# Kernel optimization log

Hardware: AMD Instinct MI355X
Metric: run time of the kernel (lower is better)

## Reference

```python
import jax, jax.numpy as jnp
import numpy as np
import math

GROUPS = 32
EPS = 1e-5
NUM_HEADS = 8


def group_norm(x, gamma, beta):
    # x: [B, C, H, W]; normalize within each of GROUPS channel groups over (C/G, H, W)
    B, C, H, W = x.shape
    xg = x.reshape(B, GROUPS, C // GROUPS, H, W)
    mean = jnp.mean(xg, axis=(2, 3, 4), keepdims=True)
    var = jnp.var(xg, axis=(2, 3, 4), keepdims=True)
    xn = ((xg - mean) * jax.lax.rsqrt(var + EPS)).reshape(B, C, H, W)
    return xn * gamma[None, :, None, None] + beta[None, :, None, None]


def setup_inputs() -> dict:
    key = jax.random.key(0)
    ks = jax.random.split(key, 10)
    C = 512
    B, H, W = 2, 64, 64
    s = 1.0 / math.sqrt(C)
    return {
        "x": jax.random.normal(ks[0], (B, C, H, W), jnp.float32),
        "gamma": jnp.ones((C,), jnp.float32),
        "beta": jnp.zeros((C,), jnp.float32),
        "Wq": jax.random.normal(ks[1], (C, C), jnp.float32) * s,
        "bq": jax.random.normal(ks[2], (C,), jnp.float32) * 0.01,
        "Wk": jax.random.normal(ks[3], (C, C), jnp.float32) * s,
        "bk": jax.random.normal(ks[4], (C,), jnp.float32) * 0.01,
        "Wv": jax.random.normal(ks[5], (C, C), jnp.float32) * s,
        "bv": jax.random.normal(ks[6], (C,), jnp.float32) * 0.01,
        "Wo": jax.random.normal(ks[7], (C, C), jnp.float32) * s,
        "bo": jax.random.normal(ks[8], (C,), jnp.float32) * 0.01,
    }


def reference(x, gamma, beta, Wq, bq, Wk, bk, Wv, bv, Wo, bo):
    B, C, H, W = x.shape
    N = H * W
    hd = C // NUM_HEADS
    h = group_norm(x, gamma, beta)
    h = h.reshape(B, C, N).transpose(0, 2, 1)  # [B, N, C]
    # torch nn.Linear: y = x @ W.T + b
    q = (h @ Wq.T + bq).reshape(B, N, NUM_HEADS, hd)
    k = (h @ Wk.T + bk).reshape(B, N, NUM_HEADS, hd)
    v = (h @ Wv.T + bv).reshape(B, N, NUM_HEADS, hd)
    scale = 1.0 / math.sqrt(hd)
    attn = jnp.einsum('bihd,bjhd->bijh', q, k) * scale  # [B, N, N, heads]
    attn = jax.nn.softmax(attn, axis=2)
    o = jnp.einsum('bijh,bjhd->bihd', attn, v).reshape(B, N, C)
    o = o @ Wo.T + bo
    o = o.transpose(0, 2, 1).reshape(B, C, H, W)
    return x + o
```

## Files before the change

### kernel.cpp

```cpp
#include <hip/hip_runtime.h>
#include <cstdint>
#include <cstddef>

typedef __bf16 bf16x8 __attribute__((ext_vector_type(8)));
typedef float f32x4 __attribute__((ext_vector_type(4)));
typedef float f32x2 __attribute__((ext_vector_type(2)));
typedef float f32x16 __attribute__((ext_vector_type(16)));
typedef unsigned short ushort8 __attribute__((ext_vector_type(8)));
typedef unsigned u32x2 __attribute__((ext_vector_type(2)));
typedef float f4 __attribute__((ext_vector_type(4)));

__device__ __forceinline__ unsigned short f2bf(float f) {
    __bf16 b = (__bf16)f;
    return *(unsigned short*)&b;
}
__device__ __forceinline__ unsigned pk2bf(float a, float b) {
#if __has_builtin(__builtin_amdgcn_cvt_pk_bf16_f32)
    typedef __bf16 bf16x2v __attribute__((ext_vector_type(2)));
    bf16x2v r = __builtin_amdgcn_cvt_pk_bf16_f32(a, b);
    return *(unsigned*)&r;
#else
    __bf16 x = (__bf16)a, y = (__bf16)b;
    unsigned short ux = *(unsigned short*)&x, uy = *(unsigned short*)&y;
    return (unsigned)ux | ((unsigned)uy << 16);
#endif
}
__device__ __forceinline__ float bf2f(unsigned short u) {
    union { unsigned u; float f; } v; v.u = ((unsigned)u) << 16; return v.f;
}

#if __has_builtin(__builtin_amdgcn_exp2f)
#define EXP2(x) __builtin_amdgcn_exp2f(x)
#else
#define EXP2(x) exp2f(x)
#endif

#define GLL(g, l) __builtin_amdgcn_global_load_lds( \
    (__attribute__((address_space(1))) void*)(g), \
    (__attribute__((address_space(3))) void*)(l), 16, 0, 0)

#define CS 0.18033688011112042f

__global__ __launch_bounds__(256) void prep(
    const float* __restrict__ wq, const float* __restrict__ wk,
    const float* __restrict__ wv, const float* __restrict__ wo,
    unsigned short* __restrict__ wb,
    const float* __restrict__ x, float* __restrict__ part)
{
    const int bid = blockIdx.x;
    if (bid < 4096) {
        int i = bid * 256 + threadIdx.x;
        const float* src = (i < 262144) ? wq : (i < 524288) ? wk : (i < 786432) ? wv : wo;
        wb[i] = f2bf(src[i & 262143]);
        return;
    }
    const int idx = bid - 4096;
    const int q = idx & 3, bg = idx >> 2;
    const f4* xv = (const f4*)(x + (size_t)bg * 65536 + q * 16384);
    float s = 0.f, sq = 0.f;
    for (int i = threadIdx.x; i < 4096; i += 256) {
        f4 v = xv[i];
        s  += v.x + v.y + v.z + v.w;
        sq += v.x * v.x + v.y * v.y + v.z * v.z + v.w * v.w;
    }
    #pragma unroll
    for (int off = 32; off > 0; off >>= 1) {
        s  += __shfl_xor(s, off, 64);
        sq += __shfl_xor(sq, off, 64);
    }
    __shared__ float red[8];
    const int w = threadIdx.x >> 6, lane = threadIdx.x & 63;
    if (lane == 0) { red[w] = s; red[4 + w] = sq; }
    __syncthreads();
    if (threadIdx.x == 0) {
        part[(bg * 4 + q) * 2]     = red[0] + red[1] + red[2] + red[3];
        part[(bg * 4 + q) * 2 + 1] = red[4] + red[5] + red[6] + red[7];
    }
}

__global__ __launch_bounds__(256) void gn_apply(
    const float* __restrict__ x, const float* __restrict__ gamma,
    const float* __restrict__ beta, const float* __restrict__ part,
    unsigned short* __restrict__ h)
{
    const int q = blockIdx.x, bg = blockIdx.y;
    const int b = bg >> 5, g = bg & 31;
    float s = 0.f, sq = 0.f;
    #pragma unroll
    for (int j = 0; j < 4; ++j) {
        s  += part[(bg * 4 + j) * 2];
        sq += part[(bg * 4 + j) * 2 + 1];
    }
    const float mean = s * (1.f / 65536.f);
    const float rstd = rsqrtf(sq * (1.f / 65536.f) - mean * mean + 1e-5f);

    float gm[16], bt[16];
    #pragma unroll
    for (int c = 0; c < 16; ++c) {
        gm[c] = gamma[g * 16 + c] * rstd;
        bt[c] = beta[g * 16 + c];
    }
    const float* xg = x + (size_t)bg * 65536;
    const int n0 = q * 1024 + threadIdx.x * 4;
    float val[16][4];
    #pragma unroll
    for (int c = 0; c < 16; ++c) {
        f4 v = *(const f4*)&xg[(size_t)c * 4096 + n0];
        val[c][0] = (v.x - mean) * gm[c] + bt[c];
        val[c][1] = (v.y - mean) * gm[c] + bt[c];
        val[c][2] = (v.z - mean) * gm[c] + bt[c];
        val[c][3] = (v.w - mean) * gm[c] + bt[c];
    }
    #pragma unroll
    for (int nn = 0; nn < 4; ++nn) {
        ushort8 v0, v1;
        #pragma unroll
        for (int c = 0; c < 8; ++c)  v0[c]     = f2bf(val[c][nn]);
        #pragma unroll
        for (int c = 8; c < 16; ++c) v1[c - 8] = f2bf(val[c][nn]);
        unsigned short* dst = h + ((size_t)(b * 4096 + n0 + nn)) * 512 + g * 16;
        *(ushort8*)dst = v0;
        *(ushort8*)(dst + 8) = v1;
    }
}

template <int MODE, int BM>
__global__ __launch_bounds__(256, 2) void gemm_bt(
    const unsigned short* __restrict__ A,
    const unsigned short* __restrict__ Bt,
    const float* __restrict__ bias0,
    const float* __restrict__ bias1,
    const float* __restrict__ bias2,
    const float* __restrict__ resid,
    void* __restrict__ outp,
    unsigned short* __restrict__ kout,
    unsigned short* __restrict__ vtout,
    int M, int N, int K)
{
    constexpr int MT = BM / 32;
    __shared__ __attribute__((aligned(16))) unsigned short As[BM * 32];
    __shared__ __attribute__((aligned(16))) unsigned short Bs[128 * 32];
    const int t = threadIdx.x;
    const int w = t >> 6, lane = t & 63;
    const int l15 = lane & 15, l4 = lane >> 4;
    const int bm = blockIdx.y, bn = blockIdx.x;
    const int wm = (w >> 1) * (BM / 2), wn = (w & 1) * 64;

    f32x4 acc[MT][4] = {};

    const int srow = t >> 2;
    const int sc8  = (t & 3) * 8;

    const unsigned short* gA0 = A  + (size_t)(bm * BM + srow) * K + sc8;
    const unsigned short* gB0 = Bt + (size_t)(bn * 128 + srow) * K + sc8;
    const unsigned short* gB1 = gB0 + (size_t)64 * K;
    unsigned short* lA0 = &As[w * 512];
    unsigned short* lB0 = &Bs[w * 512];
    unsigned short* lB1 = &Bs[2048 + w * 512];

    for (int k0 = 0; k0 < K; k0 += 32) {
        __syncthreads();
        GLL(gA0 + k0, lA0);
        if (BM == 128) GLL(gA0 + (size_t)64 * K + k0, &As[2048 + w * 512]);
        GLL(gB0 + k0, lB0);
        GLL(gB1 + k0, lB1);
        __syncthreads();

        bf16x8 af[MT], bfr[4];
        #pragma unroll
        for (int mt = 0; mt < MT; ++mt)
            af[mt] = *(const bf16x8*)&As[(wm + mt * 16 + l15) * 32 + l4 * 8];
        #pragma unroll
        for (int nt = 0; nt < 4; ++nt)
            bfr[nt] = *(const bf16x8*)&Bs[(wn + nt * 16 + l15) * 32 + l4 * 8];
        #pragma unroll
        for (int mt = 0; mt < MT; ++mt)
            #pragma unroll
            for (int nt = 0; nt < 4; ++nt)
                acc[mt][nt] = __builtin_amdgcn_mfma_f32_16x16x32_bf16(
                    af[mt], bfr[nt], acc[mt][nt], 0, 0, 0);
    }

    if (MODE == 0) {
        unsigned short* qout = (unsigned short*)outp;
        #pragma unroll
        for (int nt = 0; nt < 4; ++nt) {
            int col = bn * 128 + wn + nt * 16 + l15;
            const float* bp = (col < 512) ? bias0 : (col < 1024) ? bias1 : bias2;
            float bv = bp[col & 511];
            if (col < 1024) {
                unsigned short* dst = (col < 512) ? qout : kout;
                int cc = col & 511;
                float sc = (col < 512) ? CS : 1.0f;
                #pragma unroll
                for (int mt = 0; mt < MT; ++mt)
                    #pragma unroll
                    for (int r = 0; r < 4; ++r) {
                        int row = bm * BM + wm + mt * 16 + l4 * 4 + r;
                        dst[(size_t)row * 512 + cc] = f2bf((acc[mt][nt][r] + bv) * sc);
                    }
            } else {
                int hd = col - 1024;
                #pragma unroll
                for (int mt = 0; mt < MT; ++mt) {
                    int m = bm * BM + wm + mt * 16 + l4 * 4;
                    int bb = m >> 12, n = m & 4095;
                    unsigned u0 = pk2bf(acc[mt][nt][0] + bv, acc[mt][nt][1] + bv);
                    unsigned u1 = pk2bf(acc[mt][nt][2] + bv, acc[mt][nt][3] + bv);
                    unsigned short* dst = vtout +
                        ((size_t)(bb * 8 + (hd >> 6)) * 64 + (hd & 63)) * 4096 + n;
                    *(u32x2*)dst = (u32x2){u0, u1};
                }
            }
        }
    } else {
        float* outF = (float*)outp;
        #pragma unroll
        for (int mt = 0; mt < MT; ++mt)
            #pragma unroll
            for (int nt = 0; nt < 4; ++nt)
                #pragma unroll
                for (int r = 0; r < 4; ++r) {
                    int c = bm * BM + wm + mt * 16 + l4 * 4 + r;
                    int m = bn * 128 + wn + nt * 16 + l15;
                    int b = m >> 12, n = m & 4095;
                    size_t idx = ((size_t)(b * 512 + c)) * 4096 + n;
                    outF[idx] = acc[mt][nt][r] + bias0[c] + resid[idx];
                }
    }
}

__global__ __launch_bounds__(256, 2) void attn_kernel(
    const unsigned short* __restrict__ qb, const unsigned short* __restrict__ kb,
    const unsigned short* __restrict__ vt,
    unsigned short* __restrict__ opart, float* __restrict__ lbuf)
{
    __shared__ __attribute__((aligned(16))) unsigned short Ks[64][72];
    __shared__ __attribute__((aligned(16))) unsigned short Vts[64][72];

    const int bh = blockIdx.y, b = bh >> 3, h = bh & 7;
    const int qbase = blockIdx.x * 256;
    const int s = blockIdx.z, ks0 = s * 2048;
    const int t = threadIdx.x, w = t >> 6, lane = t & 63;
    const int l31 = lane & 31, h5 = lane >> 5;

    const unsigned short* Qg = qb + ((size_t)(b * 4096 + qbase + w * 64)) * 512 + h * 64;
    const unsigned short* Kg = kb + ((size_t)(b * 4096 + ks0)) * 512 + h * 64;
    const unsigned short* Vg = vt + ((size_t)bh) * 64 * 4096 + ks0;

    bf16x8 qf[2][4];
    #pragma unroll
    for (int qt = 0; qt < 2; ++qt)
        #pragma unroll
        for (int kc = 0; kc < 4; ++kc)
            qf[qt][kc] = *(const bf16x8*)(Qg + (size_t)(qt * 32 + l31) * 512 + kc * 16 + h5 * 8);

    f32x16 Oacc[2][2] = {};
    float li[2] = {0.f, 0.f};

    const int sr = t >> 2, sc = (t & 3) * 16;
    const int grp = (sr >> 2) & 3;
    const int srcrow = (grp == 1) ? sr + 4 : (grp == 2) ? sr - 4 : sr;
    const unsigned short* gK = Kg + (size_t)srcrow * 512 + sc;
    const unsigned short* gV = Vg + (size_t)sr * 4096 + sc;
    unsigned short* lK = &Ks[sr][sc];
    unsigned short* lV = &Vts[sr][sc];

    ushort8 kr[2], vr[2];
    kr[0] = *(const ushort8*)(gK);
    kr[1] = *(const ushort8*)(gK + 8);
    vr[0] = *(const ushort8*)(gV);
    vr[1] = *(const ushort8*)(gV + 8);

    for (int kt = 0; kt < 32; ++kt) {
        __syncthreads();
        *(ushort8*)(lK)     = kr[0];
        *(ushort8*)(lK + 8) = kr[1];
        *(ushort8*)(lV)     = vr[0];
        *(ushort8*)(lV + 8) = vr[1];
        __syncthreads();
        if (kt < 31) {
            const unsigned short* nk = gK + (size_t)(kt + 1) * 64 * 512;
            const unsigned short* nv = gV + (kt + 1) * 64;
            kr[0] = *(const ushort8*)(nk);
            kr[1] = *(const ushort8*)(nk + 8);
            vr[0] = *(const ushort8*)(nv);
            vr[1] = *(const ushort8*)(nv + 8);
        }

        f32x16 St[2][2] = {};
        #pragma unroll
        for (int ct = 0; ct < 2; ++ct)
            #pragma unroll
            for (int kc = 0; kc < 4; ++kc) {
                bf16x8 kf = *(const bf16x8*)&Ks[ct * 32 + l31][kc * 16 + h5 * 8];
                St[0][ct] = __builtin_amdgcn_mfma_f32_32x32x16_bf16(kf, qf[0][kc], St[0][ct], 0, 0, 0);
                St[1][ct] = __builtin_amdgcn_mfma_f32_32x32x16_bf16(kf, qf[1][kc], St[1][ct], 0, 0, 0);
            }

        union PU { unsigned u[4]; bf16x8 v; };
        PU pf[2][4];
        #pragma unroll
        for (int qt = 0; qt < 2; ++qt) {
            f32x2 a2 = {0.f, 0.f};
            #pragma unroll
            for (int ct = 0; ct < 2; ++ct) {
                #pragma unroll
                for (int r = 0; r < 16; ++r)
                    St[qt][ct][r] = EXP2(St[qt][ct][r]);
                #pragma unroll
                for (int r = 0; r < 8; ++r) {
                    f32x2 p = {St[qt][ct][2 * r], St[qt][ct][2 * r + 1]};
                    a2 += p;
                }
                #pragma unroll
                for (int kkl = 0; kkl < 2; ++kkl)
                    #pragma unroll
                    for (int i = 0; i < 4; ++i)
                        pf[qt][ct * 2 + kkl].u[i] =
                            pk2bf(St[qt][ct][kkl * 8 + 2 * i], St[qt][ct][kkl * 8 + 2 * i + 1]);
            }
            li[qt] += a2[0] + a2[1];
        }

        #pragma unroll
        for (int kkl = 0; kkl < 4; ++kkl)
            #pragma unroll
            for (int dt = 0; dt < 2; ++dt) {
                bf16x8 vf = *(const bf16x8*)&Vts[dt * 32 + l31][kkl * 16 + h5 * 8];
                Oacc[dt][0] = __builtin_amdgcn_mfma_f32_32x32x16_bf16(vf, pf[0][kkl].v, Oacc[dt][0], 0, 0, 0);
                Oacc[dt][1] = __builtin_amdgcn_mfma_f32_32x32x16_bf16(vf, pf[1][kkl].v, Oacc[dt][1], 0, 0, 0);
            }
    }

    #pragma unroll
    for (int qt = 0; qt < 2; ++qt) {
        float lf = li[qt] + __shfl_xor(li[qt], 32, 64);
        size_t qrow = ((size_t)s * 16 + bh) * 4096 + qbase + w * 64 + qt * 32 + l31;
        if (h5 == 0) lbuf[qrow] = lf;
        unsigned short* orow = opart + qrow * 64;
        #pragma unroll
        for (int dt = 0; dt < 2; ++dt)
            #pragma unroll
            for (int p = 0; p < 8; ++p) {
                int d = dt * 32 + 2 * (p & 1) + 8 * (p >> 1) + 4 * h5;
                unsigned u = pk2bf(Oacc[dt][qt][2 * p], Oacc[dt][qt][2 * p + 1]);
                *(unsigned*)(orow + d) = u;
            }
    }
}

__global__ __launch_bounds__(256) void combine_o(
    const unsigned short* __restrict__ opart, const float* __restrict__ lbuf,
    unsigned short* __restrict__ o)
{
    int gid = blockIdx.x * 256 + threadIdx.x;
    int row = gid >> 3, c8 = gid & 7;
    int bh = row >> 12, q = row & 4095;
    int b = bh >> 3, h = bh & 7;
    float inv = 1.f / (lbuf[row] + lbuf[65536 + row]);
    ushort8 o0 = *(const ushort8*)(opart + (size_t)row * 64 + c8 * 8);
    ushort8 o1 = *(const ushort8*)(opart + ((size_t)65536 + row) * 64 + c8 * 8);
    ushort8 r;
    #pragma unroll
    for (int i = 0; i < 8; ++i)
        r[i] = f2bf((bf2f(o0[i]) + bf2f(o1[i])) * inv);
    *(ushort8*)(o + ((size_t)(b * 4096 + q)) * 512 + h * 64 + c8 * 8) = r;
}

extern "C" void kernel_launch(void* const* d_in, const int* in_sizes, int n_in,
                              void* d_out, int out_size, void* d_ws, size_t ws_size,
                              hipStream_t stream) {
    const float* x     = (const float*)d_in[0];
    const float* gamma = (const float*)d_in[1];
    const float* beta  = (const float*)d_in[2];
    const float* Wq    = (const float*)d_in[3];
    const float* bq    = (const float*)d_in[4];
    const float* Wk    = (const float*)d_in[5];
    const float* bk    = (const float*)d_in[6];
    const float* Wv    = (const float*)d_in[7];
    const float* bv    = (const float*)d_in[8];
    const float* Wo    = (const float*)d_in[9];
    const float* bo    = (const float*)d_in[10];
    float* out = (float*)d_out;

    char* ws = (char*)d_ws;
    const size_t MB = 1024 * 1024;
    unsigned short* qbuf   = (unsigned short*)(ws);
    unsigned short* kbuf   = (unsigned short*)(ws + 8 * MB);
    unsigned short* obuf   = kbuf;
    unsigned short* vtb    = (unsigned short*)(ws + 16 * MB);
    unsigned short* h      = (unsigned short*)(ws + 24 * MB);
    unsigned short* opart  = (unsigned short*)(ws + 24 * MB);
    unsigned short* wb     = (unsigned short*)(ws + 56 * MB);
    float*          gnpart = (float*)(ws + 58 * MB);
    float*          lbuf   = (float*)(ws + 58 * MB + 256 * 1024);

    prep<<<dim3(4352), dim3(256), 0, stream>>>(Wq, Wk, Wv, Wo, wb, x, gnpart);
    gn_apply<<<dim3(4, 64), dim3(256), 0, stream>>>(x, gamma, beta, gnpart, h);

    gemm_bt<0, 128><<<dim3(12, 64), dim3(256), 0, stream>>>(
        h, wb, bq, bk, bv, nullptr, qbuf, kbuf, vtb, 8192, 1536, 512);

    attn_kernel<<<dim3(16, 16, 2), dim3(256), 0, stream>>>(qbuf, kbuf, vtb, opart, lbuf);
    combine_o<<<dim3(2048), dim3(256), 0, stream>>>(opart, lbuf, obuf);

    gemm_bt<1, 64><<<dim3(64, 8), dim3(256), 0, stream>>>(
        wb + 786432, obuf, bo, nullptr, nullptr, x, out, nullptr, nullptr, 512, 8192, 512);
}
```

Measured before the change: 224.8 us.

## Fuse split-K attention combine into output projection GEMM B-tile load

Removes the separate combine_o kernel. The output GEMM now reads both attention partials and the row sums directly, normalizing while staging its B tile into LDS. The attention epilogue stages O through shared memory so global stores are coalesced 16-byte rows. This saves a launch and an intermediate buffer write/read, but the combine work is repeated for every M-block and the B load becomes synchronous register-path loads instead of direct-to-LDS.

```diff
diff --git a/kernel.cpp b/kernel.cpp
--- a/kernel.cpp
+++ b/kernel.cpp
@@ -135,6 +135,7 @@
     void* __restrict__ outp,
     unsigned short* __restrict__ kout,
     unsigned short* __restrict__ vtout,
+    const float* __restrict__ lbufp,
     int M, int N, int K)
 {
     constexpr int MT = BM / 32;
@@ -151,19 +152,45 @@
     const int srow = t >> 2;
     const int sc8  = (t & 3) * 8;
 
-    const unsigned short* gA0 = A  + (size_t)(bm * BM + srow) * K + sc8;
+    const unsigned short* gA0 = A + (size_t)(bm * BM + srow) * K + sc8;
+    unsigned short* lA0 = &As[w * 512];
+
     const unsigned short* gB0 = Bt + (size_t)(bn * 128 + srow) * K + sc8;
     const unsigned short* gB1 = gB0 + (size_t)64 * K;
-    unsigned short* lA0 = &As[w * 512];
     unsigned short* lB0 = &Bs[w * 512];
     unsigned short* lB1 = &Bs[2048 + w * 512];
+
+    const int r0 = bn * 128 + srow, r1 = r0 + 64;
+    const int b0r = r0 >> 12, q0r = r0 & 4095;
+    const int b1r = r1 >> 12, q1r = r1 & 4095;
 
     for (int k0 = 0; k0 < K; k0 += 32) {
         __syncthreads();
         GLL(gA0 + k0, lA0);
         if (BM == 128) GLL(gA0 + (size_t)64 * K + k0, &As[2048 + w * 512]);
-        GLL(gB0 + k0, lB0);
-        GLL(gB1 + k0, lB1);
+        if (MODE == 0) {
+            GLL(gB0 + k0, lB0);
+            GLL(gB1 + k0, lB1);
+        } else {
+            const int c = k0 + sc8;
+            const int hh = c >> 6, dd = c & 63;
+            const size_t row0 = ((size_t)(b0r * 8 + hh) << 12) + q0r;
+            const size_t row1 = ((size_t)(b1r * 8 + hh) << 12) + q1r;
+            ushort8 p00 = *(const ushort8*)(Bt + row0 * 64 + dd);
+            ushort8 p01 = *(const ushort8*)(Bt + (row0 + 65536) * 64 + dd);
+            ushort8 p10 = *(const ushort8*)(Bt + row1 * 64 + dd);
+            ushort8 p11 = *(const ushort8*)(Bt + (row1 + 65536) * 64 + dd);
+            float inv0 = 1.f / (lbufp[row0] + lbufp[row0 + 65536]);
+            float inv1 = 1.f / (lbufp[row1] + lbufp[row1 + 65536]);
+            ushort8 c0, c1;
+            #pragma unroll
+            for (int i = 0; i < 8; ++i) {
+                c0[i] = f2bf((bf2f(p00[i]) + bf2f(p01[i])) * inv0);
+                c1[i] = f2bf((bf2f(p10[i]) + bf2f(p11[i])) * inv1);
+            }
+            *(ushort8*)&Bs[t * 8] = c0;
+            *(ushort8*)&Bs[2048 + t * 8] = c1;
+        }
         __syncthreads();
 
         bf16x8 af[MT], bfr[4];
@@ -235,8 +262,10 @@
     const unsigned short* __restrict__ vt,
     unsigned short* __restrict__ opart, float* __restrict__ lbuf)
 {
-    __shared__ __attribute__((aligned(16))) unsigned short Ks[64][72];
-    __shared__ __attribute__((aligned(16))) unsigned short Vts[64][72];
+    __shared__ __attribute__((aligned(16))) unsigned short smem[256 * 72];
+    unsigned short (*Ks)[72]  = (unsigned short(*)[72])smem;
+    unsigned short (*Vts)[72] = (unsigned short(*)[72])(smem + 64 * 72);
+    unsigned short (*Oepi)[72] = (unsigned short(*)[72])smem;
 
     const int bh = blockIdx.y, b = bh >> 3, h = bh & 7;
     const int qbase = blockIdx.x * 256;
@@ -333,39 +362,28 @@
             }
     }
 
+    __syncthreads();
     #pragma unroll
     for (int qt = 0; qt < 2; ++qt) {
         float lf = li[qt] + __shfl_xor(li[qt], 32, 64);
         size_t qrow = ((size_t)s * 16 + bh) * 4096 + qbase + w * 64 + qt * 32 + l31;
         if (h5 == 0) lbuf[qrow] = lf;
-        unsigned short* orow = opart + qrow * 64;
         #pragma unroll
         for (int dt = 0; dt < 2; ++dt)
             #pragma unroll
             for (int p = 0; p < 8; ++p) {
                 int d = dt * 32 + 2 * (p & 1) + 8 * (p >> 1) + 4 * h5;
                 unsigned u = pk2bf(Oacc[dt][qt][2 * p], Oacc[dt][qt][2 * p + 1]);
-                *(unsigned*)(orow + d) = u;
-            }
-    }
-}
-
-__global__ __launch_bounds__(256) void combine_o(
-    const unsigned short* __restrict__ opart, const float* __restrict__ lbuf,
-    unsigned short* __restrict__ o)
-{
-    int gid = blockIdx.x * 256 + threadIdx.x;
-    int row = gid >> 3, c8 = gid & 7;
-    int bh = row >> 12, q = row & 4095;
-    int b = bh >> 3, h = bh & 7;
-    float inv = 1.f / (lbuf[row] + lbuf[65536 + row]);
-    ushort8 o0 = *(const ushort8*)(opart + (size_t)row * 64 + c8 * 8);
-    ushort8 o1 = *(const ushort8*)(opart + ((size_t)65536 + row) * 64 + c8 * 8);
-    ushort8 r;
-    #pragma unroll
-    for (int i = 0; i < 8; ++i)
-        r[i] = f2bf((bf2f(o0[i]) + bf2f(o1[i])) * inv);
-    *(ushort8*)(o + ((size_t)(b * 4096 + q)) * 512 + h * 64 + c8 * 8) = r;
+                *(unsigned*)&Oepi[w * 64 + qt * 32 + l31][d] = u;
+            }
+    }
+    unsigned short* Og = opart +
+        (((size_t)s * 16 + bh) * 4096 + qbase + w * 64) * 64;
+    #pragma unroll
+    for (int c8 = 0; c8 < 8; ++c8) {
+        ushort8 val = *(const ushort8*)&Oepi[w * 64 + lane][c8 * 8];
+        *(ushort8*)(Og + (size_t)lane * 64 + c8 * 8) = val;
+    }
 }
 
 extern "C" void kernel_launch(void* const* d_in, const int* in_sizes, int n_in,
@@ -386,25 +404,25 @@
 
     char* ws = (char*)d_ws;
     const size_t MB = 1024 * 1024;
+    const size_t KB = 1024;
     unsigned short* qbuf   = (unsigned short*)(ws);
-    unsigned short* kbuf   = (unsigned short*)(ws + 8 * MB);
-    unsigned short* obuf   = kbuf;
-    unsigned short* vtb    = (unsigned short*)(ws + 16 * MB);
-    unsigned short* h      = (unsigned short*)(ws + 24 * MB);
-    unsigned short* opart  = (unsigned short*)(ws + 24 * MB);
-    unsigned short* wb     = (unsigned short*)(ws + 56 * MB);
-    float*          gnpart = (float*)(ws + 58 * MB);
-    float*          lbuf   = (float*)(ws + 58 * MB + 256 * 1024);
+    unsigned short* kbuf   = (unsigned short*)(ws + 8 * MB + 64 * KB);
+    unsigned short* vtb    = (unsigned short*)(ws + 16 * MB + 192 * KB);
+    unsigned short* h      = (unsigned short*)(ws + 24 * MB + 320 * KB);
+    unsigned short* opart  = (unsigned short*)(ws + 33 * MB);
+    unsigned short* wb     = (unsigned short*)(ws + 49 * MB + 64 * KB);
+    float*          gnpart = (float*)(ws + 51 * MB + 128 * KB);
+    float*          lbuf   = (float*)(ws + 51 * MB + 192 * KB);
 
     prep<<<dim3(4352), dim3(256), 0, stream>>>(Wq, Wk, Wv, Wo, wb, x, gnpart);
     gn_apply<<<dim3(4, 64), dim3(256), 0, stream>>>(x, gamma, beta, gnpart, h);
 
     gemm_bt<0, 128><<<dim3(12, 64), dim3(256), 0, stream>>>(
-        h, wb, bq, bk, bv, nullptr, qbuf, kbuf, vtb, 8192, 1536, 512);
+        h, wb, bq, bk, bv, nullptr, qbuf, kbuf, vtb, nullptr, 8192, 1536, 512);
 
     attn_kernel<<<dim3(16, 16, 2), dim3(256), 0, stream>>>(qbuf, kbuf, vtb, opart, lbuf);
-    combine_o<<<dim3(2048), dim3(256), 0, stream>>>(opart, lbuf, obuf);
 
     gemm_bt<1, 64><<<dim3(64, 8), dim3(256), 0, stream>>>(
-        wb + 786432, obuf, bo, nullptr, nullptr, x, out, nullptr, nullptr, 512, 8192, 512);
-}
+        wb + 786432, opart, bo, nullptr, nullptr, x, out, nullptr, nullptr,
+        lbuf, 512, 8192, 512);
+}
```

After: 234.5 us. +4.3%, slower.
